# Kernel optimization log

Measured on AMD Instinct MI355X. Metric: run time of the kernel, lower is better.

Reference implementation:

```python
import jax, jax.numpy as jnp
import numpy as np

COST_CLASS, COST_MASK, COST_DICE = 1.0, 1.0, 1.0
ALPHA, GAMMA = 0.25, 2.0


def setup_inputs() -> dict:
    key = jax.random.key(0)
    k1, k2, k3, k4 = jax.random.split(key, 4)
    B, Q, C, H, W, T, Hm, Wm = 2, 100, 134, 256, 256, 20, 512, 512
    return {
        "masks_queries_logits": jax.random.normal(k1, (B, Q, H, W), jnp.float32),
        "class_queries_logits": jax.random.normal(k2, (B, Q, C), jnp.float32),
        "mask_labels": jax.random.uniform(k3, (B, T, Hm, Wm), dtype=jnp.float32),
        "class_labels": jax.random.randint(k4, (B, T), 0, C),
    }


def _nearest_resize(x, H, W):
    # torch F.interpolate(mode='nearest'): src_idx = floor(dst_idx * in / out)
    Hi, Wi = x.shape[-2], x.shape[-1]
    ri = (jnp.arange(H) * Hi) // H
    ci = (jnp.arange(W) * Wi) // W
    return x[..., ri, :][..., ci]


def _cost_matrices(masks_queries_logits, class_queries_logits, mask_labels, class_labels):
    B, Q, H, W = masks_queries_logits.shape
    HW = H * W
    tgt = _nearest_resize(mask_labels, H, W)                       # [B,T,H,W]
    probs = jax.nn.softmax(class_queries_logits, axis=-1)          # [B,Q,C]
    # cost_class = -probs[:, labels]  -> [B,Q,T]
    cost_class = -jnp.take_along_axis(
        probs, jnp.broadcast_to(class_labels[:, None, :], (B, Q, class_labels.shape[1])), axis=2
    )
    x = masks_queries_logits.reshape(B, Q, HW)                     # [B,Q,HW]
    lab = tgt.reshape(B, -1, HW)                                   # [B,T,HW]
    p = jax.nn.sigmoid(x)
    ce_pos = jax.nn.softplus(-x)   # BCEWithLogits(target=1)
    ce_neg = jax.nn.softplus(x)    # BCEWithLogits(target=0)
    focal_pos = ALPHA * (1.0 - p) ** GAMMA * ce_pos
    focal_neg = (1.0 - ALPHA) * p ** GAMMA * ce_neg
    cost_mask = (jnp.einsum('bqk,btk->bqt', focal_pos, lab)
                 + jnp.einsum('bqk,btk->bqt', focal_neg, 1.0 - lab)) / HW
    numer = 2.0 * jnp.einsum('bqk,btk->bqt', p, lab)
    denom = p.sum(-1)[:, :, None] + lab.sum(-1)[:, None, :]
    cost_dice = 1.0 - (numer + 1.0) / (denom + 1.0)
    return COST_MASK * cost_mask + COST_CLASS * cost_class + COST_DICE * cost_dice


def _hungarian(cost):
    # Exact O(n^3) Hungarian (Jonker-Volgenant style potentials), numpy on host.
    # Zero-pads to square like the torch code; dummy cols all-zero so the real
    # assignment equals the rectangular optimum.
    n_rows, n_cols = cost.shape
    n = max(n_rows, n_cols)
    a = np.zeros((n + 1, n + 1), dtype=np.float64)
    a[1:n_rows + 1, 1:n_cols + 1] = cost
    u = np.zeros(n + 1); v = np.zeros(n + 1)
    p = np.zeros(n + 1, dtype=np.int64)
    way = np.zeros(n + 1, dtype=np.int64)
    for i in range(1, n + 1):
        p[0] = i; j0 = 0
        minv = np.full(n + 1, np.inf)
        used = np.zeros(n + 1, dtype=bool)
        while True:
            used[j0] = True
            i0 = p[j0]
            cur = a[i0, 1:] - u[i0] - v[1:]
            free = ~used[1:]
            upd = free & (cur < minv[1:])
            minv[1:][upd] = cur[upd]
            way[1:][upd] = j0
            cand = np.where(free, minv[1:], np.inf)
            j1 = int(np.argmin(cand)) + 1
            delta = cand[j1 - 1]
            u[p[used]] += delta
            v[used] -= delta
            minv[1:][free] -= delta
            j0 = j1
            if p[j0] == 0:
                break
        while j0:
            j1 = way[j0]
            p[j0] = p[j1]
            j0 = j1
    rows, cols = [], []
    for j in range(1, n_cols + 1):
        r = p[j] - 1
        if 0 <= r < n_rows:
            rows.append(r); cols.append(j - 1)
    rows = np.asarray(rows, dtype=np.int64)
    cols = np.asarray(cols, dtype=np.int64)
    order = np.argsort(rows)  # torch impl emits pairs in ascending row order
    return rows[order], cols[order]


def reference(masks_queries_logits, class_queries_logits, mask_labels, class_labels):
    cost = _cost_matrices(masks_queries_logits, class_queries_logits, mask_labels, class_labels)
    cost_np = np.asarray(jax.device_get(cost), dtype=np.float64)  # [B,Q,T]
    pairs = [np.stack(_hungarian(c)) for c in cost_np]            # each [2, min(Q,T)]
    return jnp.asarray(np.stack(pairs), dtype=jnp.int32)          # [B, 2, T]
```

## Files before the change

kernel.cpp:

```cpp
#include <hip/hip_runtime.h>
#include <hip/hip_bf16.h>
#include <math.h>

#define HW_   65536
#define B_    2
#define Q_    100
#define C_    134
#define T_    20
#define NHUN  100
#define MT_   7
#define KSB   128
#define BKCH  512
#define WKCH  128
#define PREC  1088

typedef __attribute__((ext_vector_type(8))) short bf16x8;
typedef __attribute__((ext_vector_type(4))) float f32x4;

#define LABPS_OFF  0
#define CC_OFF     512
#define COST_OFF   4608
#define BASE_END   8704
#define LABT_HI_F  BASE_END
#define PART_OFF   (LABT_HI_F + 1310720)
#define CSUM_OFF   (PART_OFF + B_ * KSB * MT_ * PREC)
#define WS_END_F   (CSUM_OFF + B_ * MT_ * 1056)

__device__ inline unsigned short f2bf(float f) {
    unsigned int u = __builtin_bit_cast(unsigned int, f);
    u += 0x7FFFu + ((u >> 16) & 1u);
    return (unsigned short)(u >> 16);
}
__device__ inline float softplusf(float x) {
    float ax = fabsf(x);
    return fmaxf(x, 0.0f) + log1pf(expf(-ax));
}

__global__ void lab_prep_kernel(const float* __restrict__ ml, unsigned short* __restrict__ labT,
                                float* __restrict__ lab_ps, int writeT) {
    int b = blockIdx.x, t = blockIdx.y, ksl = blockIdx.z;
    int tid = threadIdx.x;
    const float* src = ml + (size_t)(b * T_ + t) * 262144;
    size_t dst = ((size_t)(b * T_ + t)) << 16;
    float acc = 0.f;
    for (int it = 0; it < 8; ++it) {
        int k = ksl * 8192 + it * 1024 + tid * 4;
        int r = k >> 8, c = k & 255;
        const float* s = src + r * 1024 + 2 * c;
        float4 u = *(const float4*)s;
        float4 w = *(const float4*)(s + 4);
        float v[4] = {u.x, u.z, w.x, w.z};
        unsigned short h[4];
#pragma unroll
        for (int e = 0; e < 4; ++e) { h[e] = f2bf(v[e]); acc += v[e]; }
        if (writeT) *(ushort4*)(labT + dst + k) = make_ushort4(h[0], h[1], h[2], h[3]);
    }
    for (int off = 32; off > 0; off >>= 1) acc += __shfl_down(acc, off);
    __shared__ float sb[4];
    int wid = tid >> 6, lane = tid & 63;
    if (lane == 0) sb[wid] = acc;
    __syncthreads();
    if (tid == 0) lab_ps[(b * T_ + t) * 8 + ksl] = sb[0] + sb[1] + sb[2] + sb[3];
}

__global__ void class_cost_kernel(const float* __restrict__ cl, const int* __restrict__ labels,
                                  float* __restrict__ cc) {
    int bq  = blockIdx.x;
    int b   = bq / Q_;
    int tid = threadIdx.x;
    __shared__ float sl[C_];
    const float* src = cl + (size_t)bq * C_;
    for (int c = tid; c < C_; c += 64) sl[c] = src[c];
    __syncthreads();
    float mx = -INFINITY;
    for (int c = tid; c < C_; c += 64) mx = fmaxf(mx, sl[c]);
    for (int off = 32; off > 0; off >>= 1) mx = fmaxf(mx, __shfl_xor(mx, off));
    float se = 0.f;
    for (int c = tid; c < C_; c += 64) se += expf(sl[c] - mx);
    for (int off = 32; off > 0; off >>= 1) se += __shfl_xor(se, off);
    float inv = 1.0f / se;
    if (tid < T_) {
        int lbl = labels[b * T_ + tid];
        cc[bq * T_ + tid] = -expf(sl[lbl] - mx) * inv;
    }
}

__global__ __launch_bounds__(256) void focal_mfma_kernel(
        const float* __restrict__ mq, const unsigned short* __restrict__ labT,
        float* __restrict__ part) {
    int idx = blockIdx.x;
    int mt  = idx % MT_;
    int rem = idx / MT_;
    int ks  = rem % KSB;
    int b   = rem / KSB;
    int tid  = threadIdx.x;
    int wave = tid >> 6, lane = tid & 63;
    int lg = lane >> 4, lr = lane & 15;

    int q = mt * 16 + lr;
    bool qok = (q < Q_);
    const float* xrow = mq + ((size_t)(b * Q_ + (qok ? q : 0)) << 16);
    int koff = ks * BKCH + wave * WKCH + lg * 8;

    const unsigned short* b1 = labT + (((size_t)(b * T_ + lr)) << 16);
    const unsigned short* b2 = labT + (((size_t)(b * T_ + 16 + (lr & 3))) << 16);
    bool n2row = (lr < 4);

    f32x4 accD0 = {0,0,0,0}, accD1 = {0,0,0,0};
    f32x4 accP0 = {0,0,0,0}, accP1 = {0,0,0,0};
    float F = 0.f, P = 0.f;

    bf16x8 zer;
#pragma unroll
    for (int e = 0; e < 8; ++e) zer[e] = 0;

    for (int kk = 0; kk < 4; ++kk) {
        int kb = koff + kk * 32;
        float4 u0 = *(const float4*)(xrow + kb);
        float4 u1 = *(const float4*)(xrow + kb + 4);
        float xv[8] = {u0.x, u0.y, u0.z, u0.w, u1.x, u1.y, u1.z, u1.w};

        bf16x8 f1 = *(const bf16x8*)(b1 + kb);
        bf16x8 f2 = n2row ? *(const bf16x8*)(b2 + kb) : zer;

        bf16x8 dh, ph;
#pragma unroll
        for (int e = 0; e < 8; ++e) {
            float x  = xv[e];
            float ax = fabsf(x);
            float a  = __expf(-ax);
            float rr = 1.0f / (1.0f + a);
            float p  = (x >= 0.f) ? rr : a * rr;
            float om = (x >= 0.f) ? a * rr : rr;
            float l1 = __logf(1.0f + a);
            float spn = fmaxf(-x, 0.f) + l1;
            float spp = spn + x;
            float fp = 0.25f * om * om * spn;
            float fn = 0.75f * p * p * spp;
            F += fn; P += p;
            dh[e] = (short)f2bf(fp - fn);
            ph[e] = (short)f2bf(p);
        }
        accD0 = __builtin_amdgcn_mfma_f32_16x16x32_bf16(dh, f1, accD0, 0, 0, 0);
        accD1 = __builtin_amdgcn_mfma_f32_16x16x32_bf16(dh, f2, accD1, 0, 0, 0);
        accP0 = __builtin_amdgcn_mfma_f32_16x16x32_bf16(ph, f1, accP0, 0, 0, 0);
        accP1 = __builtin_amdgcn_mfma_f32_16x16x32_bf16(ph, f2, accP1, 0, 0, 0);
    }

    F += __shfl_down(F, 32); F += __shfl_down(F, 16);
    P += __shfl_down(P, 32); P += __shfl_down(P, 16);

    __shared__ float red[4][4][64][4];
    __shared__ float fpb[4][2][16];
#pragma unroll
    for (int r = 0; r < 4; ++r) {
        red[wave][0][lane][r] = accD0[r];
        red[wave][1][lane][r] = accD1[r];
        red[wave][2][lane][r] = accP0[r];
        red[wave][3][lane][r] = accP1[r];
    }
    if (lane < 16) { fpb[wave][0][lane] = F; fpb[wave][1][lane] = P; }
    __syncthreads();
    for (int e = tid; e < 1024; e += 256) {
        int f  = e >> 8;
        int l2 = (e & 255) >> 2;
        int r  = e & 3;
        part[(size_t)idx * PREC + e] =
            red[0][f][l2][r] + red[1][f][l2][r] + red[2][f][l2][r] + red[3][f][l2][r];
    }
    if (tid < 16)
        part[(size_t)idx * PREC + 1024 + tid] =
            fpb[0][0][tid] + fpb[1][0][tid] + fpb[2][0][tid] + fpb[3][0][tid];
    else if (tid < 32) {
        int l = tid - 16;
        part[(size_t)idx * PREC + 1040 + l] =
            fpb[0][1][l] + fpb[1][1][l] + fpb[2][1][l] + fpb[3][1][l];
    }
}

__global__ __launch_bounds__(256) void reduce_part_kernel(const float* __restrict__ part,
                                                          float* __restrict__ Csum) {
    int bm   = blockIdx.x;
    int mt   = bm % MT_;
    int b    = bm / MT_;
    int tid  = threadIdx.x;
    int epos = tid & 31;
    int grp  = tid >> 5;
    int e    = blockIdx.y * 32 + epos;

    const float* base = part + (size_t)((b * KSB) * MT_ + mt) * PREC + e;
    float s = 0.f;
    for (int k = 0; k < 16; ++k) {
        s += base[(size_t)(grp * 16 + k) * MT_ * PREC];
    }
    __shared__ float red[8][33];
    red[grp][epos] = s;
    __syncthreads();
    if (tid < 32) {
        float tot = 0.f;
        for (int g = 0; g < 8; ++g) tot += red[g][tid];
        Csum[(size_t)bm * 1056 + e] = tot;
    }
}

__global__ void compose_kernel(const float* __restrict__ Csum, const float* __restrict__ cc,
                               const float* __restrict__ lab_ps, float* __restrict__ cost) {
    int bm = blockIdx.x;
    int mt = bm % MT_;
    int b  = bm / MT_;
    int tid = threadIdx.x;
    const float* C = Csum + (size_t)bm * 1056;
    int qm = tid / T_, t = tid % T_;
    int q = mt * 16 + qm;
    if (qm < 16 && q < Q_) {
        int nt   = t >> 4;
        int lane = ((qm >> 2) << 4) | (t & 15);
        int reg  = qm & 3;
        float Sd = C[(0 + nt) * 256 + lane * 4 + reg];
        float Sp = C[(2 + nt) * 256 + lane * 4 + reg];
        float F  = C[1024 + qm];
        float P  = C[1040 + qm];
        float L = 0.f;
        for (int s8 = 0; s8 < 8; ++s8) L += lab_ps[(b * T_ + t) * 8 + s8];
        float cm = (Sd + F) * (1.0f / (float)HW_);
        float cd = 1.0f - (2.0f * Sp + 1.0f) / (P + L + 1.0f);
        cost[(b * Q_ + q) * T_ + t] = cm + cd + cc[(b * Q_ + q) * T_ + t];
    }
}

__global__ __launch_bounds__(1024) void mask_cost_mono_kernel(
        const float* __restrict__ mq, const float* __restrict__ ml,
        const float* __restrict__ cc, const float* __restrict__ lab_ps,
        float* __restrict__ cost) {
    int bq  = blockIdx.x;
    int b   = bq / Q_;
    int tid = threadIdx.x;
    const float* xb  = mq + (size_t)bq * HW_;
    const float* mlb = ml + (size_t)b * T_ * 262144;
    float s1[T_], s2[T_];
#pragma unroll
    for (int t = 0; t < T_; ++t) { s1[t] = 0.f; s2[t] = 0.f; }
    float F = 0.f, P = 0.f;
    for (int k = tid; k < HW_; k += 1024) {
        int i = k >> 8, j = k & 255;
        float x = xb[k];
        float p = 1.0f / (1.0f + expf(-x));
        float spn = softplusf(-x);
        float spp = softplusf(x);
        float om = 1.0f - p;
        float fp = 0.25f * om * om * spn;
        float fn = 0.75f * p * p * spp;
        F += fn; P += p;
        float diff = fp - fn;
        int off0 = i * 1024 + 2 * j;
#pragma unroll
        for (int t = 0; t < T_; ++t) {
            float lab = mlb[t * 262144 + off0];
            s1[t] = fmaf(diff, lab, s1[t]);
            s2[t] = fmaf(p,    lab, s2[t]);
        }
    }
    __shared__ float sbuf[16][42];
    int wid = tid >> 6, lane = tid & 63;
#pragma unroll
    for (int t = 0; t < T_; ++t) {
        for (int off = 32; off > 0; off >>= 1) {
            s1[t] += __shfl_down(s1[t], off);
            s2[t] += __shfl_down(s2[t], off);
        }
    }
    for (int off = 32; off > 0; off >>= 1) { F += __shfl_down(F, off); P += __shfl_down(P, off); }
    if (lane == 0) {
#pragma unroll
        for (int t = 0; t < T_; ++t) { sbuf[wid][t] = s1[t]; sbuf[wid][T_ + t] = s2[t]; }
        sbuf[wid][40] = F; sbuf[wid][41] = P;
    }
    __syncthreads();
    if (tid < T_) {
        float S1 = 0.f, S2 = 0.f, Fs = 0.f, Ps = 0.f;
        for (int w = 0; w < 16; ++w) {
            S1 += sbuf[w][tid]; S2 += sbuf[w][T_ + tid];
            Fs += sbuf[w][40];  Ps += sbuf[w][41];
        }
        float L = 0.f;
        for (int sl = 0; sl < 8; ++sl) L += lab_ps[(b * T_ + tid) * 8 + sl];
        float cm = (S1 + Fs) * (1.0f / (float)HW_);
        float cd = 1.0f - (2.0f * S2 + 1.0f) / (Ps + L + 1.0f);
        cost[bq * T_ + tid] = cm + cd + cc[bq * T_ + tid];
    }
}

__global__ __launch_bounds__(64) void hungarian_kernel(const float* __restrict__ cost,
                                                       int* __restrict__ out) {
    int b    = blockIdx.x;
    int lane = threadIdx.x;

    __shared__ float  csh[Q_ * T_];
    __shared__ double u[T_ + 1];
    __shared__ int    p[NHUN + 1];
    __shared__ int    way[NHUN + 1];

    for (int idx = lane; idx < Q_ * T_; idx += 64) csh[idx] = cost[b * Q_ * T_ + idx];
    for (int j = lane; j <= NHUN; j += 64) { p[j] = 0; way[j] = 0; }
    if (lane <= T_) u[lane] = 0.0;
    __syncthreads();

    const int ja = lane;
    const int jb = lane + 64;
    const bool jb_ok = (jb <= NHUN);
    double v_a = 0.0, v_b = 0.0;

    for (int i = 1; i <= T_; ++i) {
        if (lane == 0) p[0] = i;
        double m_a = INFINITY, m_b = INFINITY;
        bool us_a = false, us_b = false;
        __syncthreads();
        int j0 = 0;
        while (true) {
            if (ja == j0) us_a = true;
            if (jb == j0) us_b = true;
            int    i0  = p[j0];
            double ui0 = u[i0];
            double cand = INFINITY; int candj = 0x7fffffff;
            if (!us_a && ja >= 1) {
                double cur = (double)csh[(ja - 1) * T_ + (i0 - 1)] - ui0 - v_a;
                if (cur < m_a) { m_a = cur; way[ja] = j0; }
                cand = m_a; candj = ja;
            }
            if (jb_ok && !us_b) {
                double cur = (double)csh[(jb - 1) * T_ + (i0 - 1)] - ui0 - v_b;
                if (cur < m_b) { m_b = cur; way[jb] = j0; }
                if (m_b < cand || (m_b == cand && jb < candj)) { cand = m_b; candj = jb; }
            }
            for (int off = 32; off > 0; off >>= 1) {
                double ov = __shfl_xor(cand, off);
                int    oj = __shfl_xor(candj, off);
                if (ov < cand || (ov == cand && oj < candj)) { cand = ov; candj = oj; }
            }
            double delta = cand; int j1 = candj;
            if (us_a) { u[p[ja]] += delta; v_a -= delta; } else { m_a -= delta; }
            if (jb_ok) {
                if (us_b) { u[p[jb]] += delta; v_b -= delta; } else { m_b -= delta; }
            }
            j0 = j1;
            __syncthreads();
            if (p[j0] == 0) break;
        }
        if (lane == 0) {
            int jj = j0;
            while (jj) { int jn = way[jj]; p[jj] = p[jn]; jj = jn; }
        }
        __syncthreads();
    }

    if (lane == 0) {
        int* ob = out + b * 2 * T_;
        int k = 0;
        for (int j = 1; j <= NHUN; ++j) {
            if (p[j] != 0) { ob[k] = j - 1; ob[T_ + k] = p[j] - 1; ++k; }
        }
    }
}

extern "C" void kernel_launch(void* const* d_in, const int* in_sizes, int n_in,
                              void* d_out, int out_size, void* d_ws, size_t ws_size,
                              hipStream_t stream) {
    const float* mq     = (const float*)d_in[0];
    const float* cl     = (const float*)d_in[1];
    const float* ml     = (const float*)d_in[2];
    const int*   labels = (const int*)d_in[3];
    int* out = (int*)d_out;
    float* ws = (float*)d_ws;

    float* lab_ps = ws + LABPS_OFF;
    float* cc     = ws + CC_OFF;
    float* cost   = ws + COST_OFF;

    size_t need = (size_t)WS_END_F * 4;

    if (ws_size >= need) {
        unsigned short* labT = (unsigned short*)(ws + LABT_HI_F);
        float* part = ws + PART_OFF;
        float* Csum = ws + CSUM_OFF;
        hipLaunchKernelGGL(lab_prep_kernel,   dim3(B_, T_, 8), dim3(256), 0, stream,
                           ml, labT, lab_ps, 1);
        hipLaunchKernelGGL(class_cost_kernel, dim3(B_ * Q_),   dim3(64),  0, stream, cl, labels, cc);
        hipLaunchKernelGGL(focal_mfma_kernel, dim3(B_ * KSB * MT_), dim3(256), 0, stream,
                           mq, labT, part);
        hipLaunchKernelGGL(reduce_part_kernel, dim3(B_ * MT_, 33), dim3(256), 0, stream,
                           part, Csum);
        hipLaunchKernelGGL(compose_kernel,    dim3(B_ * MT_),  dim3(320), 0, stream,
                           Csum, cc, lab_ps, cost);
    } else {
        hipLaunchKernelGGL(lab_prep_kernel,   dim3(B_, T_, 8), dim3(256), 0, stream,
                           ml, (unsigned short*)ws, lab_ps, 0);
        hipLaunchKernelGGL(class_cost_kernel, dim3(B_ * Q_),   dim3(64),  0, stream, cl, labels, cc);
        hipLaunchKernelGGL(mask_cost_mono_kernel, dim3(B_ * Q_), dim3(1024), 0, stream,
                           mq, ml, cc, lab_ps, cost);
    }
    hipLaunchKernelGGL(hungarian_kernel, dim3(B_), dim3(64), 0, stream, cost, out);
}
```

Before: 79.07 us.

## Fuse class softmax into compose; make Hungarian single-wave float with ballot argmin

Folds the class-cost softmax into the compose kernel, so one launch and one workspace round trip disappear from the fast path. The Hungarian kernel moves from double to float potentials. Its shuffle-based argmin with index tie-breaking becomes a min reduction followed by a ballot/ffs to find the lowest index. The per-iteration __syncthreads is replaced by a block fence, which relies on the block being a single 64-lane wave. Float potentials can change the chosen assignment when costs are near ties, compared with the double-precision reference.

```diff
diff --git a/kernel.cpp b/kernel.cpp
--- a/kernel.cpp
+++ b/kernel.cpp
@@ -203,16 +203,39 @@
     }
 }
 
-__global__ void compose_kernel(const float* __restrict__ Csum, const float* __restrict__ cc,
-                               const float* __restrict__ lab_ps, float* __restrict__ cost) {
+__global__ __launch_bounds__(320) void compose_kernel(
+        const float* __restrict__ Csum, const float* __restrict__ cl,
+        const int* __restrict__ labels, const float* __restrict__ lab_ps,
+        float* __restrict__ cost) {
     int bm = blockIdx.x;
     int mt = bm % MT_;
     int b  = bm / MT_;
     int tid = threadIdx.x;
-    const float* C = Csum + (size_t)bm * 1056;
+    int q0 = mt * 16;
+
+    __shared__ float sl[16][136];
+    __shared__ float mx[16], se[16];
+    __shared__ int   lbl[T_];
+    for (int e = tid; e < 16 * C_; e += 320) {
+        int qm = e / C_, c = e % C_;
+        int q = q0 + qm;
+        sl[qm][c] = (q < Q_) ? cl[(size_t)(b * Q_ + q) * C_ + c] : 0.f;
+    }
+    if (tid < T_) lbl[tid] = labels[b * T_ + tid];
+    __syncthreads();
+    if (tid < 16) {
+        float m = -INFINITY;
+        for (int c = 0; c < C_; ++c) m = fmaxf(m, sl[tid][c]);
+        float s = 0.f;
+        for (int c = 0; c < C_; ++c) s += expf(sl[tid][c] - m);
+        mx[tid] = m; se[tid] = s;
+    }
+    __syncthreads();
+
     int qm = tid / T_, t = tid % T_;
-    int q = mt * 16 + qm;
+    int q = q0 + qm;
     if (qm < 16 && q < Q_) {
+        const float* C = Csum + (size_t)bm * 1056;
         int nt   = t >> 4;
         int lane = ((qm >> 2) << 4) | (t & 15);
         int reg  = qm & 3;
@@ -222,9 +245,10 @@
         float P  = C[1040 + qm];
         float L = 0.f;
         for (int s8 = 0; s8 < 8; ++s8) L += lab_ps[(b * T_ + t) * 8 + s8];
+        float ccv = -expf(sl[qm][lbl[t]] - mx[qm]) / se[qm];
         float cm = (Sd + F) * (1.0f / (float)HW_);
         float cd = 1.0f - (2.0f * Sp + 1.0f) / (P + L + 1.0f);
-        cost[(b * Q_ + q) * T_ + t] = cm + cd + cc[(b * Q_ + q) * T_ + t];
+        cost[(size_t)(b * Q_ + q) * T_ + t] = cm + cd + ccv;
     }
 }
 
@@ -295,55 +319,58 @@
     int b    = blockIdx.x;
     int lane = threadIdx.x;
 
-    __shared__ float  csh[Q_ * T_];
-    __shared__ double u[T_ + 1];
-    __shared__ int    p[NHUN + 1];
-    __shared__ int    way[NHUN + 1];
+    __shared__ float csh[Q_ * T_];
+    __shared__ float u[T_ + 1];
+    __shared__ int   p[NHUN + 1];
+    __shared__ int   way[NHUN + 1];
 
     for (int idx = lane; idx < Q_ * T_; idx += 64) csh[idx] = cost[b * Q_ * T_ + idx];
     for (int j = lane; j <= NHUN; j += 64) { p[j] = 0; way[j] = 0; }
-    if (lane <= T_) u[lane] = 0.0;
+    if (lane <= T_) u[lane] = 0.f;
     __syncthreads();
 
     const int ja = lane;
     const int jb = lane + 64;
     const bool jb_ok = (jb <= NHUN);
-    double v_a = 0.0, v_b = 0.0;
+    float v_a = 0.f, v_b = 0.f;
 
     for (int i = 1; i <= T_; ++i) {
         if (lane == 0) p[0] = i;
-        double m_a = INFINITY, m_b = INFINITY;
+        float m_a = INFINITY, m_b = INFINITY;
         bool us_a = false, us_b = false;
         __syncthreads();
         int j0 = 0;
         while (true) {
             if (ja == j0) us_a = true;
             if (jb == j0) us_b = true;
-            int    i0  = p[j0];
-            double ui0 = u[i0];
-            double cand = INFINITY; int candj = 0x7fffffff;
-            if (!us_a && ja >= 1) {
-                double cur = (double)csh[(ja - 1) * T_ + (i0 - 1)] - ui0 - v_a;
+            int   i0  = p[j0];
+            float ui0 = u[i0];
+            bool fa = (!us_a && ja >= 1);
+            bool fb = (jb_ok && !us_b);
+            if (fa) {
+                float cur = csh[(ja - 1) * T_ + (i0 - 1)] - ui0 - v_a;
                 if (cur < m_a) { m_a = cur; way[ja] = j0; }
-                cand = m_a; candj = ja;
             }
-            if (jb_ok && !us_b) {
-                double cur = (double)csh[(jb - 1) * T_ + (i0 - 1)] - ui0 - v_b;
+            if (fb) {
+                float cur = csh[(jb - 1) * T_ + (i0 - 1)] - ui0 - v_b;
                 if (cur < m_b) { m_b = cur; way[jb] = j0; }
-                if (m_b < cand || (m_b == cand && jb < candj)) { cand = m_b; candj = jb; }
             }
-            for (int off = 32; off > 0; off >>= 1) {
-                double ov = __shfl_xor(cand, off);
-                int    oj = __shfl_xor(candj, off);
-                if (ov < cand || (ov == cand && oj < candj)) { cand = ov; candj = oj; }
-            }
-            double delta = cand; int j1 = candj;
+            float ca = fa ? m_a : INFINITY;
+            float cb = fb ? m_b : INFINITY;
+            float vmin = fminf(ca, cb);
+            for (int off = 32; off > 0; off >>= 1)
+                vmin = fminf(vmin, __shfl_xor(vmin, off));
+            unsigned long long ba = __ballot(ca == vmin);
+            int j1;
+            if (ba) j1 = __ffsll(ba) - 1;
+            else    j1 = __ffsll(__ballot(cb == vmin)) - 1 + 64;
+            float delta = vmin;
             if (us_a) { u[p[ja]] += delta; v_a -= delta; } else { m_a -= delta; }
             if (jb_ok) {
                 if (us_b) { u[p[jb]] += delta; v_b -= delta; } else { m_b -= delta; }
             }
+            __threadfence_block();
             j0 = j1;
-            __syncthreads();
             if (p[j0] == 0) break;
         }
         if (lane == 0) {
@@ -384,13 +411,12 @@
         float* Csum = ws + CSUM_OFF;
         hipLaunchKernelGGL(lab_prep_kernel,   dim3(B_, T_, 8), dim3(256), 0, stream,
                            ml, labT, lab_ps, 1);
-        hipLaunchKernelGGL(class_cost_kernel, dim3(B_ * Q_),   dim3(64),  0, stream, cl, labels, cc);
         hipLaunchKernelGGL(focal_mfma_kernel, dim3(B_ * KSB * MT_), dim3(256), 0, stream,
                            mq, labT, part);
         hipLaunchKernelGGL(reduce_part_kernel, dim3(B_ * MT_, 33), dim3(256), 0, stream,
                            part, Csum);
         hipLaunchKernelGGL(compose_kernel,    dim3(B_ * MT_),  dim3(320), 0, stream,
-                           Csum, cc, lab_ps, cost);
+                           Csum, cl, labels, lab_ps, cost);
     } else {
         hipLaunchKernelGGL(lab_prep_kernel,   dim3(B_, T_, 8), dim3(256), 0, stream,
                            ml, (unsigned short*)ws, lab_ps, 0);
```

After: 77.01 us. -2.6%, faster.
